# Performance work log

Hardware: AMD Instinct MI355X
Metric: run time of the kernel (lower is better)

The kernel has to match this reference:

```python
import jax, jax.numpy as jnp
import numpy as np

N_NODES = 50000
N_EDGES = 800000
D = 128
BN_EPS = 1e-5


def setup_inputs() -> dict:
    key = jax.random.key(0)
    k1, k2, k3, k4 = jax.random.split(key, 4)
    feature = jax.random.normal(k1, (N_NODES, D), dtype=jnp.float32)
    W = jax.random.normal(k2, (D, D), dtype=jnp.float32) * (1.0 / np.sqrt(D))
    b = jnp.zeros((D,), dtype=jnp.float32)
    gamma = jnp.ones((D,), dtype=jnp.float32)
    beta = jnp.zeros((D,), dtype=jnp.float32)
    src = jax.random.randint(k3, (N_EDGES,), 0, N_NODES, dtype=jnp.int64)
    dst = jax.random.randint(k4, (N_EDGES,), 0, N_NODES, dtype=jnp.int64)
    return {"feature": feature, "W": W, "b": b, "gamma": gamma, "beta": beta,
            "src": src, "dst": dst}


def reference(feature, W, b, gamma, beta, src, dst):
    # --- message passing: copy_u + mean over in-neighbors ---
    n = feature.shape[0]
    msgs = feature[src]  # [E, D] gather of source node features
    agg = jax.ops.segment_sum(msgs, dst, num_segments=n)  # [N, D]
    deg = jax.ops.segment_sum(jnp.ones((src.shape[0],), feature.dtype), dst,
                              num_segments=n)  # [N]
    h = jnp.where(deg[:, None] > 0, agg / jnp.maximum(deg, 1.0)[:, None], 0.0)
    # --- node apply: linear ---
    h = h @ W.T + b
    # --- BatchNorm1d (training mode: biased batch stats over node dim) ---
    mu = jnp.mean(h, axis=0)
    var = jnp.mean(jnp.square(h - mu), axis=0)
    h = (h - mu) / jnp.sqrt(var + BN_EPS) * gamma + beta
    # --- activation + residual (dropout p=0 is identity) ---
    h = jax.nn.relu(h)
    h = feature + h
    return h
```

## Files before the change

### kernel.cpp

```cpp
#include <hip/hip_runtime.h>
#include <cstddef>
#include <cstdint>

#define N_NODES 50000
#define N_EDGES 800000
#define D 128
#define BN_EPS 1e-5f

#define NBUCKET 782
#define BCAP 1536
#define PART_BLOCKS 256
#define PART_CHUNK 3125
#define SLOTS 48
#define SLOTS_P 50
#define GEMM_CHUNKS 1563
#define GEMM_GRID   512
#define FEAT_V8     (N_NODES * D / 8)
#define SLICE_V8    (N_NODES * 4)
#define W_V8        (D * D / 8)
#define CAST_BLOCKS ((FEAT_V8 + W_V8 + 255) / 256)
#define ZERO_V4     3704

typedef __attribute__((ext_vector_type(8))) short short8_t;
typedef __attribute__((ext_vector_type(8))) unsigned short u16x8;
typedef __attribute__((ext_vector_type(4))) float f32x4;
typedef __attribute__((ext_vector_type(4))) int i32x4;

#define WS_STAT_OFF    0
#define WS_STAT8_OFF   1024
#define WS_GCUR_OFF    9216
#define WS_WB_OFF      59264
#define WS_CLAIM_OFF   92032
#define WS_HB_OFF      4896640
#define WS_H2_OFF      17696640
#define WS_FB_OFF      30496640

static __device__ __forceinline__ unsigned short f2bf(float x) {
    unsigned u = __float_as_uint(x);
    unsigned r = (u + 0x7fffu + ((u >> 16) & 1u)) >> 16;
    return (unsigned short)r;
}
static __device__ __forceinline__ float bf2f(unsigned short v) {
    return __uint_as_float(((unsigned)v) << 16);
}

__global__ __launch_bounds__(256) void prezero_k(i32x4* __restrict__ zws) {
    int i = blockIdx.x * 256 + threadIdx.x;
    if (i < ZERO_V4) zws[i] = (i32x4){0, 0, 0, 0};
}

__global__ __launch_bounds__(256) void castpart_k(const float* __restrict__ feat,
                                                  const float* __restrict__ W,
                                                  u16x8* __restrict__ fb,
                                                  u16x8* __restrict__ wb,
                                                  const int* __restrict__ src,
                                                  const int* __restrict__ dst,
                                                  int* __restrict__ gcur,
                                                  unsigned* __restrict__ claims) {
    __shared__ unsigned pk[PART_CHUNK];
    __shared__ int hist[NBUCKET];
    __shared__ int base_l[NBUCKET];
    const int t = threadIdx.x;

    if (blockIdx.x < PART_BLOCKS) {
        const int base = blockIdx.x * PART_CHUNK;

        for (int b = t; b < NBUCKET; b += 256) hist[b] = 0;
        __syncthreads();

        for (int i = t; i < PART_CHUNK; i += 256) {
            int s = __builtin_nontemporal_load(src + base + i);
            int d = __builtin_nontemporal_load(dst + base + i);
            pk[i] = ((unsigned)s << 16) | (unsigned)d;
            atomicAdd(&hist[d >> 6], 1);
        }
        __syncthreads();

        for (int b = t; b < NBUCKET; b += 256) {
            int h = hist[b];
            base_l[b] = h ? atomicAdd(gcur + b * 16, h) : 0;
            hist[b] = 0;
        }
        __syncthreads();

        for (int i = t; i < PART_CHUNK; i += 256) {
            unsigned u = pk[i];
            int bkt = (int)(u & 0xffffu) >> 6;
            int k = atomicAdd(&hist[bkt], 1);
            int pos = base_l[bkt] + k;
            if (pos < BCAP) claims[bkt * BCAP + pos] = u;
        }
    } else {
        int i = (blockIdx.x - PART_BLOCKS) * 256 + t;
        if (i < FEAT_V8) {
            int q  = i / SLICE_V8;
            int r  = i - q * SLICE_V8;
            int n  = r >> 2, oc = r & 3;
            const f32x4* fp = reinterpret_cast<const f32x4*>(feat + n * D + q * 32 + oc * 8);
            f32x4 x0 = __builtin_nontemporal_load(fp);
            f32x4 x1 = __builtin_nontemporal_load(fp + 1);
            u16x8 o;
            o[0] = f2bf(x0.x); o[1] = f2bf(x0.y); o[2] = f2bf(x0.z); o[3] = f2bf(x0.w);
            o[4] = f2bf(x1.x); o[5] = f2bf(x1.y); o[6] = f2bf(x1.z); o[7] = f2bf(x1.w);
            __builtin_nontemporal_store(o, fb + i);
        } else if (i < FEAT_V8 + W_V8) {
            int j = i - FEAT_V8;
            const f32x4* fp = reinterpret_cast<const f32x4*>(W) + j * 2;
            f32x4 x0 = __builtin_nontemporal_load(fp);
            f32x4 x1 = __builtin_nontemporal_load(fp + 1);
            u16x8 o;
            o[0] = f2bf(x0.x); o[1] = f2bf(x0.y); o[2] = f2bf(x0.z); o[3] = f2bf(x0.w);
            o[4] = f2bf(x1.x); o[5] = f2bf(x1.y); o[6] = f2bf(x1.z); o[7] = f2bf(x1.w);
            __builtin_nontemporal_store(o, wb + j);
        }
    }
}

__global__ __launch_bounds__(256) void bingather_k(const int* __restrict__ gcur,
                                                   const unsigned* __restrict__ claims,
                                                   const u16x8* __restrict__ fb,
                                                   u16x8* __restrict__ hb) {
    __shared__ unsigned short ebl[64 * SLOTS_P];
    __shared__ int lcnt[64];
    const int t = threadIdx.x;
    const int b = blockIdx.x >> 2;
    const int q = blockIdx.x & 3;
    const u16x8* fbq = fb + (size_t)q * SLICE_V8;

    if (t < 64) lcnt[t] = 0;
    __syncthreads();

    const int n = min(gcur[b * 16], BCAP);
    const unsigned* cp = claims + b * BCAP;
    for (int i = t; i < n; i += 256) {
        unsigned u = cp[i];
        int dl = (int)(u & 63u);
        int k = atomicAdd(&lcnt[dl], 1);
        if (k < SLOTS) ebl[dl * SLOTS_P + k] = (unsigned short)(u >> 16);
    }
    __syncthreads();

    const int nl = t >> 2;
    const int oc = t & 3;
    const int node = (b << 6) + nl;
    const int deg = lcnt[nl];
    const int nd  = min(deg, SLOTS);
    const unsigned short* slots = ebl + nl * SLOTS_P;

    float a[8];
#pragma unroll
    for (int i = 0; i < 8; ++i) a[i] = 0.f;

    int e = 0;
    for (; e + 8 <= nd; e += 8) {
        int s0 = slots[e],     s1 = slots[e + 1];
        int s2 = slots[e + 2], s3 = slots[e + 3];
        int s4 = slots[e + 4], s5 = slots[e + 5];
        int s6 = slots[e + 6], s7 = slots[e + 7];
        u16x8 v0 = fbq[s0 * 4 + oc];
        u16x8 v1 = fbq[s1 * 4 + oc];
        u16x8 v2 = fbq[s2 * 4 + oc];
        u16x8 v3 = fbq[s3 * 4 + oc];
        u16x8 v4 = fbq[s4 * 4 + oc];
        u16x8 v5 = fbq[s5 * 4 + oc];
        u16x8 v6 = fbq[s6 * 4 + oc];
        u16x8 v7 = fbq[s7 * 4 + oc];
#pragma unroll
        for (int i = 0; i < 8; ++i)
            a[i] += ((bf2f(v0[i]) + bf2f(v1[i])) + (bf2f(v2[i]) + bf2f(v3[i]))) +
                    ((bf2f(v4[i]) + bf2f(v5[i])) + (bf2f(v6[i]) + bf2f(v7[i])));
    }
    for (; e < nd; ++e) {
        u16x8 v0 = fbq[(int)slots[e] * 4 + oc];
#pragma unroll
        for (int i = 0; i < 8; ++i) a[i] += bf2f(v0[i]);
    }

    if (node < N_NODES) {
        float inv = (deg > 0) ? 1.f / (float)deg : 0.f;
        u16x8 o;
#pragma unroll
        for (int i = 0; i < 8; ++i) o[i] = f2bf(a[i] * inv);
        hb[(size_t)q * SLICE_V8 + node * 4 + oc] = o;
    }
}

__global__ __launch_bounds__(256) void gemm_mfma_k(const u16x8* __restrict__ hb,
                                                   const u16x8* __restrict__ wb,
                                                   const float* __restrict__ bias,
                                                   unsigned short* __restrict__ h2,
                                                   float* __restrict__ colsum8,
                                                   float* __restrict__ colsumsq8) {
    const int wave = threadIdx.x >> 6;
    const int lane = threadIdx.x & 63;
    const int wm = wave >> 1, wn = wave & 1;
    const int l15 = lane & 15, l4 = lane >> 4;

    short8_t bf[4][4];
#pragma unroll
    for (int t = 0; t < 4; ++t) {
        const int col = wn * 64 + t * 16 + l15;
#pragma unroll
        for (int s = 0; s < 4; ++s) {
            u16x8 w = wb[col * 16 + s * 4 + l4];
            short8_t b8;
#pragma unroll
            for (int i = 0; i < 8; ++i) b8[i] = (short)w[i];
            bf[t][s] = b8;
        }
    }
    float bc[4];
#pragma unroll
    for (int t = 0; t < 4; ++t) bc[t] = bias[wn * 64 + t * 16 + l15];

    float s1[4] = {0.f, 0.f, 0.f, 0.f};
    float s2[4] = {0.f, 0.f, 0.f, 0.f};

    for (int chunk = blockIdx.x; chunk < GEMM_CHUNKS; chunk += gridDim.x) {
        const int rbase = chunk * 32 + wm * 16;
        const int arow = min(rbase + l15, N_NODES - 1);
        short8_t af[4];
#pragma unroll
        for (int s = 0; s < 4; ++s) {
            u16x8 hv8 = hb[(size_t)s * SLICE_V8 + arow * 4 + l4];
            short8_t t8;
#pragma unroll
            for (int i = 0; i < 8; ++i) t8[i] = (short)hv8[i];
            af[s] = t8;
        }

        f32x4 acc[4];
#pragma unroll
        for (int t = 0; t < 4; ++t) acc[t] = (f32x4){0.f, 0.f, 0.f, 0.f};

#pragma unroll
        for (int s = 0; s < 4; ++s)
#pragma unroll
            for (int t = 0; t < 4; ++t)
                acc[t] = __builtin_amdgcn_mfma_f32_16x16x32_bf16(af[s], bf[t][s],
                                                                 acc[t], 0, 0, 0);

        const int orow0 = rbase + l4 * 4;
#pragma unroll
        for (int t = 0; t < 4; ++t) {
            const int col = wn * 64 + t * 16 + l15;
#pragma unroll
            for (int r = 0; r < 4; ++r) {
                const int row = orow0 + r;
                if (row < N_NODES) {
                    float hv = acc[t][r] + bc[t];
                    h2[(size_t)row * D + col] = f2bf(hv);
                    s1[t] += hv;
                    s2[t] += hv * hv;
                }
            }
        }
    }

#pragma unroll
    for (int t = 0; t < 4; ++t) {
        s1[t] += __shfl_xor(s1[t], 16); s1[t] += __shfl_xor(s1[t], 32);
        s2[t] += __shfl_xor(s2[t], 16); s2[t] += __shfl_xor(s2[t], 32);
    }
    if (lane < 16) {
        const int sh = (blockIdx.x & 7) * 128;
#pragma unroll
        for (int t = 0; t < 4; ++t) {
            int col = wn * 64 + t * 16 + lane;
            atomicAdd(colsum8 + sh + col, s1[t]);
            atomicAdd(colsumsq8 + sh + col, s2[t]);
        }
    }
}

__global__ __launch_bounds__(256) void statreduce_k(const float* __restrict__ colsum8,
                                                    const float* __restrict__ colsumsq8,
                                                    float* __restrict__ colsum,
                                                    float* __restrict__ colsumsq) {
    int t = threadIdx.x;
    const float* src = (t < 128) ? colsum8 : colsumsq8;
    float* dst = (t < 128) ? colsum : colsumsq;
    int c = t & 127;
    float s = 0.f;
#pragma unroll
    for (int k = 0; k < 8; ++k) s += src[k * 128 + c];
    dst[c] = s;
}

__global__ __launch_bounds__(256) void epilogue_k(const u16x8* __restrict__ h2v,
                                                  const float* __restrict__ feat,
                                                  const float* __restrict__ colsum,
                                                  const float* __restrict__ colsumsq,
                                                  const float* __restrict__ gamma,
                                                  const float* __restrict__ beta,
                                                  float* __restrict__ out) {
    int idx = blockIdx.x * 256 + threadIdx.x;
    if (idx >= FEAT_V8) return;
    const int colb = (idx * 8) & 127;
    const float inv_n = 1.0f / N_NODES;

    u16x8 hv8 = h2v[idx];
    const float4* fp = reinterpret_cast<const float4*>(feat) + idx * 2;
    float4 fv0 = fp[0], fv1 = fp[1];
    float4 o0, o1;
#pragma unroll
    for (int i = 0; i < 8; ++i) {
        int c = colb + i;
        float mu  = colsum[c] * inv_n;
        float var = colsumsq[c] * inv_n - mu * mu;
        float a   = gamma[c] * rsqrtf(var + BN_EPS);
        float bb  = beta[c] - mu * a;
        float hv  = bf2f(hv8[i]);
        float fv  = (i < 4) ? (&fv0.x)[i] : (&fv1.x)[i - 4];
        float ov  = fv + fmaxf(hv * a + bb, 0.f);
        if (i < 4) (&o0.x)[i] = ov; else (&o1.x)[i - 4] = ov;
    }
    float4* op = reinterpret_cast<float4*>(out) + idx * 2;
    op[0] = o0;
    op[1] = o1;
}

extern "C" void kernel_launch(void* const* d_in, const int* in_sizes, int n_in,
                              void* d_out, int out_size, void* d_ws, size_t ws_size,
                              hipStream_t stream) {
    const float* feature = (const float*)d_in[0];
    const float* W       = (const float*)d_in[1];
    const float* b       = (const float*)d_in[2];
    const float* gamma   = (const float*)d_in[3];
    const float* beta    = (const float*)d_in[4];
    const int*   src     = (const int*)d_in[5];
    const int*   dst     = (const int*)d_in[6];
    float* out = (float*)d_out;

    char* ws = (char*)d_ws;
    float*          colsum    = (float*)(ws + WS_STAT_OFF);
    float*          colsumsq  = colsum + 128;
    float*          colsum8   = (float*)(ws + WS_STAT8_OFF);
    float*          colsumsq8 = colsum8 + 1024;
    int*            gcur      = (int*)(ws + WS_GCUR_OFF);
    u16x8*          wb        = (u16x8*)(ws + WS_WB_OFF);
    unsigned*       claims    = (unsigned*)(ws + WS_CLAIM_OFF);
    u16x8*          hb        = (u16x8*)(ws + WS_HB_OFF);
    unsigned short* h2        = (unsigned short*)(ws + WS_H2_OFF);
    u16x8*          fb        = (u16x8*)(ws + WS_FB_OFF);

    prezero_k<<<15, 256, 0, stream>>>((i32x4*)ws);
    castpart_k<<<PART_BLOCKS + CAST_BLOCKS, 256, 0, stream>>>(
        feature, W, fb, wb, src, dst, gcur, claims);
    bingather_k<<<NBUCKET * 4, 256, 0, stream>>>(gcur, claims, fb, hb);
    gemm_mfma_k<<<GEMM_GRID, 256, 0, stream>>>(hb, wb, b, h2, colsum8, colsumsq8);
    statreduce_k<<<1, 256, 0, stream>>>(colsum8, colsumsq8, colsum, colsumsq);
    epilogue_k<<<(FEAT_V8 + 255) / 256, 256, 0, stream>>>(
        (u16x8*)h2, feature, colsum, colsumsq, gamma, beta, out);
}
```

Before: 90.48 us.

## Fold BN stat reduction into epilogue and pre-reduce GEMM stats in LDS

```diff
diff --git a/kernel.cpp b/kernel.cpp
--- a/kernel.cpp
+++ b/kernel.cpp
@@ -191,6 +191,7 @@
                                                    unsigned short* __restrict__ h2,
                                                    float* __restrict__ colsum8,
                                                    float* __restrict__ colsumsq8) {
+    __shared__ float sred[2][128];
     const int wave = threadIdx.x >> 6;
     const int lane = threadIdx.x & 63;
     const int wm = wave >> 1, wn = wave & 1;
@@ -262,62 +263,80 @@
         s1[t] += __shfl_xor(s1[t], 16); s1[t] += __shfl_xor(s1[t], 32);
         s2[t] += __shfl_xor(s2[t], 16); s2[t] += __shfl_xor(s2[t], 32);
     }
-    if (lane < 16) {
-        const int sh = (blockIdx.x & 7) * 128;
+    if (lane < 16 && wm == 0) {
 #pragma unroll
         for (int t = 0; t < 4; ++t) {
             int col = wn * 64 + t * 16 + lane;
-            atomicAdd(colsum8 + sh + col, s1[t]);
-            atomicAdd(colsumsq8 + sh + col, s2[t]);
-        }
-    }
-}
-
-__global__ __launch_bounds__(256) void statreduce_k(const float* __restrict__ colsum8,
-                                                    const float* __restrict__ colsumsq8,
-                                                    float* __restrict__ colsum,
-                                                    float* __restrict__ colsumsq) {
-    int t = threadIdx.x;
-    const float* src = (t < 128) ? colsum8 : colsumsq8;
-    float* dst = (t < 128) ? colsum : colsumsq;
-    int c = t & 127;
-    float s = 0.f;
-#pragma unroll
-    for (int k = 0; k < 8; ++k) s += src[k * 128 + c];
-    dst[c] = s;
+            sred[0][col] = s1[t];
+            sred[1][col] = s2[t];
+        }
+    }
+    __syncthreads();
+    if (lane < 16 && wm == 1) {
+#pragma unroll
+        for (int t = 0; t < 4; ++t) {
+            int col = wn * 64 + t * 16 + lane;
+            sred[0][col] += s1[t];
+            sred[1][col] += s2[t];
+        }
+    }
+    __syncthreads();
+    if (lane < 16 && wm == 0) {
+        const int sh = (blockIdx.x & 7) * 128;
+#pragma unroll
+        for (int t = 0; t < 4; ++t) {
+            int col = wn * 64 + t * 16 + lane;
+            atomicAdd(colsum8 + sh + col, sred[0][col]);
+            atomicAdd(colsumsq8 + sh + col, sred[1][col]);
+        }
+    }
 }
 
 __global__ __launch_bounds__(256) void epilogue_k(const u16x8* __restrict__ h2v,
                                                   const float* __restrict__ feat,
-                                                  const float* __restrict__ colsum,
-                                                  const float* __restrict__ colsumsq,
+                                                  const float* __restrict__ colsum8,
+                                                  const float* __restrict__ colsumsq8,
                                                   const float* __restrict__ gamma,
                                                   const float* __restrict__ beta,
                                                   float* __restrict__ out) {
-    int idx = blockIdx.x * 256 + threadIdx.x;
+    __shared__ float av_l[128], bv_l[128];
+    const int t = threadIdx.x;
+    if (t < 128) {
+        const float inv_n = 1.0f / N_NODES;
+        float s1 = 0.f, s2 = 0.f;
+#pragma unroll
+        for (int k = 0; k < 8; ++k) {
+            s1 += colsum8[k * 128 + t];
+            s2 += colsumsq8[k * 128 + t];
+        }
+        float mu  = s1 * inv_n;
+        float var = s2 * inv_n - mu * mu;
+        float a   = gamma[t] * rsqrtf(var + BN_EPS);
+        av_l[t] = a;
+        bv_l[t] = beta[t] - mu * a;
+    }
+    __syncthreads();
+
+    int idx = blockIdx.x * 256 + t;
     if (idx >= FEAT_V8) return;
     const int colb = (idx * 8) & 127;
-    const float inv_n = 1.0f / N_NODES;
 
     u16x8 hv8 = h2v[idx];
-    const float4* fp = reinterpret_cast<const float4*>(feat) + idx * 2;
-    float4 fv0 = fp[0], fv1 = fp[1];
-    float4 o0, o1;
+    const f32x4* fp = reinterpret_cast<const f32x4*>(feat) + idx * 2;
+    f32x4 fv0 = __builtin_nontemporal_load(fp);
+    f32x4 fv1 = __builtin_nontemporal_load(fp + 1);
+    f32x4 o0, o1;
 #pragma unroll
     for (int i = 0; i < 8; ++i) {
         int c = colb + i;
-        float mu  = colsum[c] * inv_n;
-        float var = colsumsq[c] * inv_n - mu * mu;
-        float a   = gamma[c] * rsqrtf(var + BN_EPS);
-        float bb  = beta[c] - mu * a;
-        float hv  = bf2f(hv8[i]);
-        float fv  = (i < 4) ? (&fv0.x)[i] : (&fv1.x)[i - 4];
-        float ov  = fv + fmaxf(hv * a + bb, 0.f);
-        if (i < 4) (&o0.x)[i] = ov; else (&o1.x)[i - 4] = ov;
-    }
-    float4* op = reinterpret_cast<float4*>(out) + idx * 2;
-    op[0] = o0;
-    op[1] = o1;
+        float hv = bf2f(hv8[i]);
+        float fv = (i < 4) ? fv0[i] : fv1[i - 4];
+        float ov = fv + fmaxf(hv * av_l[c] + bv_l[c], 0.f);
+        if (i < 4) o0[i] = ov; else o1[i - 4] = ov;
+    }
+    f32x4* op = reinterpret_cast<f32x4*>(out) + idx * 2;
+    __builtin_nontemporal_store(o0, op);
+    __builtin_nontemporal_store(o1, op + 1);
 }
 
 extern "C" void kernel_launch(void* const* d_in, const int* in_sizes, int n_in,
@@ -333,8 +352,6 @@
     float* out = (float*)d_out;
 
     char* ws = (char*)d_ws;
-    float*          colsum    = (float*)(ws + WS_STAT_OFF);
-    float*          colsumsq  = colsum + 128;
     float*          colsum8   = (float*)(ws + WS_STAT8_OFF);
     float*          colsumsq8 = colsum8 + 1024;
     int*            gcur      = (int*)(ws + WS_GCUR_OFF);
@@ -349,7 +366,6 @@
         feature, W, fb, wb, src, dst, gcur, claims);
     bingather_k<<<NBUCKET * 4, 256, 0, stream>>>(gcur, claims, fb, hb);
     gemm_mfma_k<<<GEMM_GRID, 256, 0, stream>>>(hb, wb, b, h2, colsum8, colsumsq8);
-    statreduce_k<<<1, 256, 0, stream>>>(colsum8, colsumsq8, colsum, colsumsq);
     epilogue_k<<<(FEAT_V8 + 255) / 256, 256, 0, stream>>>(
-        (u16x8*)h2, feature, colsum, colsumsq, gamma, beta, out);
-}
+        (u16x8*)h2, feature, colsum8, colsumsq8, gamma, beta, out);
+}
```

New measurement: 89.24 us. About the same (-1.4%).
